# Optimization experiments

Hardware: AMD Instinct MI355X
Metric: run time of the kernel (lower is better)

Reference implementation:

```python
import jax, jax.numpy as jnp
import numpy as np

K = 131072
C = 128
THR = 9.2885e-30


def setup_inputs() -> dict:
    key = jax.random.key(0)
    k1, k2, k3, k4, k5 = jax.random.split(key, 5)
    scores1 = jax.random.normal(k1, (K, C), dtype=jnp.float32)
    scores2 = jax.random.normal(k2, (K, C), dtype=jnp.float32)
    # Build lineages hitting the three supported branches, never the
    # unsupported overlapping-but-unequal case (which raises in torch).
    c1 = jax.random.randint(k3, (K,), 0, C)
    off = jax.random.randint(k4, (K,), 1, C)
    c2 = (c1 + off) % C  # guaranteed != c1
    case = jax.random.randint(k5, (K,), 0, 3)  # 0: equal 1-hot, 1: equal 2-hot, 2: disjoint 1-hots
    oh1 = jax.nn.one_hot(c1, C, dtype=jnp.int32)
    oh2 = jax.nn.one_hot(c2, C, dtype=jnp.int32)
    is1 = (case == 1)[:, None]
    is2 = (case == 2)[:, None]
    Y1 = oh1 + jnp.where(is1, oh2, 0)
    Y2 = jnp.where(is2, oh2, Y1)
    return {"scores1": scores1, "Y1": Y1, "scores2": scores2, "Y2": Y2}


def reference(scores1, Y1, scores2, Y2):
    P1 = jax.nn.softmax(scores1, axis=1)  # [K, C]
    P2 = jax.nn.softmax(scores2, axis=1)
    L1 = Y1.astype(P1.dtype)
    L2 = Y2.astype(P2.dtype)

    eq = jnp.all(Y1 == Y2, axis=1)
    s = jnp.sum(Y1, axis=1)
    case1 = eq & (s == 1)   # equal one-hot lineage
    case2 = eq & (s == 2)   # equal two-hot lineage

    nclass = scores1.shape[1]
    rows = jnp.arange(scores1.shape[0])
    idx_a = jnp.argmax(Y1, axis=1)                      # first nonzero
    idx_b = nclass - 1 - jnp.argmax(Y1[:, ::-1], axis=1)  # last nonzero
    p1a = P1[rows, idx_a]; p1b = P1[rows, idx_b]
    p2a = P2[rows, idx_a]; p2b = P2[rows, idx_b]

    def safe_neglog(p):
        return jnp.where(p > THR, -jnp.log(jnp.maximum(p, THR)), 0.0)

    # case1: -log P1[i,c] - log P2[i,c] (each term thresholded)
    loss1 = safe_neglog(p1a) + safe_neglog(p2a)

    # case2: split two-hot into l1 (first pos), l2 (second pos); both one-hot
    # so disjunction == gathered prob.
    prob2 = 1.0 - (1.0 - p1a * p2b) * (1.0 - p1b * p2a)
    loss2 = safe_neglog(prob2)

    # default disjoint case: vectorized disjunction D(l,p) = 1 - prod(1 - l*p)
    D11 = 1.0 - jnp.prod(1.0 - L1 * P1, axis=1)  # Px1_Y1
    D21 = 1.0 - jnp.prod(1.0 - L2 * P1, axis=1)  # Px1_Y2
    D12 = 1.0 - jnp.prod(1.0 - L1 * P2, axis=1)  # Px2_Y1
    D22 = 1.0 - jnp.prod(1.0 - L2 * P2, axis=1)  # Px2_Y2
    probd = 1.0 - (1.0 - D11 * D22) * (1.0 - D21 * D12)
    lossd = safe_neglog(probd)

    return jnp.where(case1, loss1, jnp.where(case2, loss2, lossd))
```

## Files before the change

kernel.cpp:

```cpp
#include <hip/hip_runtime.h>


constexpr int KROWS = 131072;
constexpr int CC    = 128;
#define THRF 9.2885e-30f

__device__ __forceinline__ float hredsumf(float v){
#pragma unroll
  for (int m = 16; m > 0; m >>= 1) v += __shfl_xor(v, m, 32);
  return v;
}

__device__ __forceinline__ float neglog_safe(float p){
  return (p > THRF) ? -__logf(p) : 0.0f;
}

__device__ __forceinline__ float sel4(float p0, float p1, float p2, float p3, int s){
  float lo = (s & 1) ? p1 : p0;
  float hi = (s & 1) ? p3 : p2;
  return (s & 2) ? hi : lo;
}

__device__ __forceinline__ float gatherP(float p0, float p1, float p2, float p3, int idx){
  float c = sel4(p0, p1, p2, p3, idx & 3);
  return __shfl(c, (idx >> 2) & 31, 32);
}

__global__ __launch_bounds__(256) void wmc_loss_kernel(
    const float* __restrict__ s1, const int* __restrict__ y1,
    const float* __restrict__ s2, const int* __restrict__ y2,
    float* __restrict__ out)
{
  const int gid  = blockIdx.x * 256 + threadIdx.x;
  const int row  = gid >> 5;
  const int lane = threadIdx.x & 31;

  const size_t base = (size_t)row * CC;
  const float4 a1 = ((const float4*)(s1 + base))[lane];
  const float4 a2 = ((const float4*)(s2 + base))[lane];
  const int4   b1 = ((const int4*)(y1 + base))[lane];
  const int4   b2 = ((const int4*)(y2 + base))[lane];

  float e10 = __expf(a1.x), e11 = __expf(a1.y), e12 = __expf(a1.z), e13 = __expf(a1.w);
  float e20 = __expf(a2.x), e21 = __expf(a2.y), e22 = __expf(a2.z), e23 = __expf(a2.w);
  float inv1 = 1.0f / hredsumf(e10 + e11 + e12 + e13);
  float inv2 = 1.0f / hredsumf(e20 + e21 + e22 + e23);
  float p10 = e10 * inv1, p11 = e11 * inv1, p12 = e12 * inv1, p13 = e13 * inv1;
  float p20 = e20 * inv2, p21 = e21 * inv2, p22 = e22 * inv2, p23 = e23 * inv2;

  unsigned long long M1[4], M2[4];
  M1[0] = __ballot(b1.x); M1[1] = __ballot(b1.y); M1[2] = __ballot(b1.z); M1[3] = __ballot(b1.w);
  M2[0] = __ballot(b2.x); M2[1] = __ballot(b2.y); M2[2] = __ballot(b2.z); M2[3] = __ballot(b2.w);

  const bool hi = (threadIdx.x & 32) != 0;
  unsigned int h1[4], h2[4];
#pragma unroll
  for (int j = 0; j < 4; ++j) {
    h1[j] = hi ? (unsigned int)(M1[j] >> 32) : (unsigned int)M1[j];
    h2[j] = hi ? (unsigned int)(M2[j] >> 32) : (unsigned int)M2[j];
  }

  bool eq = (h1[0] == h2[0]) & (h1[1] == h2[1]) & (h1[2] == h2[2]) & (h1[3] == h2[3]);
  int srow = __popc(h1[0]) + __popc(h1[1]) + __popc(h1[2]) + __popc(h1[3]);

  int ia1 = 1 << 30, ib1 = -1, ia2 = 1 << 30, ib2 = -1;
#pragma unroll
  for (int j = 0; j < 4; ++j) {
    if (h1[j]) {
      ia1 = min(ia1, ((__ffs(h1[j]) - 1) << 2) + j);
      ib1 = max(ib1, ((31 - __clz(h1[j])) << 2) + j);
    }
    if (h2[j]) {
      ia2 = min(ia2, ((__ffs(h2[j]) - 1) << 2) + j);
      ib2 = max(ib2, ((31 - __clz(h2[j])) << 2) + j);
    }
  }

  float p1a1 = gatherP(p10, p11, p12, p13, ia1);
  float p1b1 = gatherP(p10, p11, p12, p13, ib1);
  float p1a2 = gatherP(p10, p11, p12, p13, ia2);
  float p1b2 = gatherP(p10, p11, p12, p13, ib2);
  float p2a1 = gatherP(p20, p21, p22, p23, ia1);
  float p2b1 = gatherP(p20, p21, p22, p23, ib1);
  float p2a2 = gatherP(p20, p21, p22, p23, ia2);
  float p2b2 = gatherP(p20, p21, p22, p23, ib2);

  float f1 = (ia1 != ib1) ? 1.0f : 0.0f;
  float f2 = (ia2 != ib2) ? 1.0f : 0.0f;
  float D11 = 1.0f - (1.0f - p1a1) * (1.0f - f1 * p1b1);
  float D12 = 1.0f - (1.0f - p2a1) * (1.0f - f1 * p2b1);
  float D21 = 1.0f - (1.0f - p1a2) * (1.0f - f2 * p1b2);
  float D22 = 1.0f - (1.0f - p2a2) * (1.0f - f2 * p2b2);

  float loss1 = neglog_safe(p1a1) + neglog_safe(p2a1);

  float prob2 = 1.0f - (1.0f - p1a1 * p2b1) * (1.0f - p1b1 * p2a1);
  float loss2 = neglog_safe(prob2);

  float probd = 1.0f - (1.0f - D11 * D22) * (1.0f - D21 * D12);
  float lossd = neglog_safe(probd);

  float loss = (eq && srow == 1) ? loss1 : (eq && srow == 2) ? loss2 : lossd;

  if (lane == 0) out[row] = loss;
}

extern "C" void kernel_launch(void* const* d_in, const int* in_sizes, int n_in,
                              void* d_out, int out_size, void* d_ws, size_t ws_size,
                              hipStream_t stream) {
  const float* s1 = (const float*)d_in[0];
  const int*   y1 = (const int*)d_in[1];
  const float* s2 = (const float*)d_in[2];
  const int*   y2 = (const int*)d_in[3];
  float* out = (float*)d_out;

  dim3 grid(KROWS / 8), block(256);
  wmc_loss_kernel<<<grid, block, 0, stream>>>(s1, y1, s2, y2, out);
}
```

Measured before the change: 232.8 us.

## Use persistent blocks with a software-prefetched row loop

The launch drops from one 8-row block per 256 threads (16384 blocks) to 2048 blocks, each looping over 8 iterations of 8 rows. The loads for the next row are issued before the current row is computed, so memory latency overlaps with compute. The aim is to cut block scheduling overhead and keep more loads in flight, at the cost of extra registers for the prefetched data and fewer, longer-lived blocks. The kernel is memory-bound and streams about 256MB, so bandwidth may already be saturated.

```diff
diff --git a/kernel.cpp b/kernel.cpp
--- a/kernel.cpp
+++ b/kernel.cpp
@@ -1,8 +1,11 @@
 #include <hip/hip_runtime.h>
 
 
-constexpr int KROWS = 131072;
-constexpr int CC    = 128;
+constexpr int KROWS       = 131072;
+constexpr int CC          = 128;
+constexpr int NB          = 2048;
+constexpr int ROWS_PER_IT = 8;
+constexpr int NIT         = KROWS / (NB * ROWS_PER_IT);
 #define THRF 9.2885e-30f
 
 __device__ __forceinline__ float hredsumf(float v){
@@ -26,21 +29,9 @@
   return __shfl(c, (idx >> 2) & 31, 32);
 }
 
-__global__ __launch_bounds__(256) void wmc_loss_kernel(
-    const float* __restrict__ s1, const int* __restrict__ y1,
-    const float* __restrict__ s2, const int* __restrict__ y2,
-    float* __restrict__ out)
+__device__ __forceinline__ float computeRow(
+    float4 a1, float4 a2, int4 b1, int4 b2, bool hi)
 {
-  const int gid  = blockIdx.x * 256 + threadIdx.x;
-  const int row  = gid >> 5;
-  const int lane = threadIdx.x & 31;
-
-  const size_t base = (size_t)row * CC;
-  const float4 a1 = ((const float4*)(s1 + base))[lane];
-  const float4 a2 = ((const float4*)(s2 + base))[lane];
-  const int4   b1 = ((const int4*)(y1 + base))[lane];
-  const int4   b2 = ((const int4*)(y2 + base))[lane];
-
   float e10 = __expf(a1.x), e11 = __expf(a1.y), e12 = __expf(a1.z), e13 = __expf(a1.w);
   float e20 = __expf(a2.x), e21 = __expf(a2.y), e22 = __expf(a2.z), e23 = __expf(a2.w);
   float inv1 = 1.0f / hredsumf(e10 + e11 + e12 + e13);
@@ -52,7 +43,6 @@
   M1[0] = __ballot(b1.x); M1[1] = __ballot(b1.y); M1[2] = __ballot(b1.z); M1[3] = __ballot(b1.w);
   M2[0] = __ballot(b2.x); M2[1] = __ballot(b2.y); M2[2] = __ballot(b2.z); M2[3] = __ballot(b2.w);
 
-  const bool hi = (threadIdx.x & 32) != 0;
   unsigned int h1[4], h2[4];
 #pragma unroll
   for (int j = 0; j < 4; ++j) {
@@ -93,16 +83,48 @@
   float D22 = 1.0f - (1.0f - p2a2) * (1.0f - f2 * p2b2);
 
   float loss1 = neglog_safe(p1a1) + neglog_safe(p2a1);
-
   float prob2 = 1.0f - (1.0f - p1a1 * p2b1) * (1.0f - p1b1 * p2a1);
   float loss2 = neglog_safe(prob2);
-
   float probd = 1.0f - (1.0f - D11 * D22) * (1.0f - D21 * D12);
   float lossd = neglog_safe(probd);
 
-  float loss = (eq && srow == 1) ? loss1 : (eq && srow == 2) ? loss2 : lossd;
+  return (eq && srow == 1) ? loss1 : (eq && srow == 2) ? loss2 : lossd;
+}
 
-  if (lane == 0) out[row] = loss;
+__global__ __launch_bounds__(256) void wmc_loss_kernel(
+    const float* __restrict__ s1, const int* __restrict__ y1,
+    const float* __restrict__ s2, const int* __restrict__ y2,
+    float* __restrict__ out)
+{
+  const int hw   = threadIdx.x >> 5;
+  const int lane = threadIdx.x & 31;
+  const bool hi  = (threadIdx.x & 32) != 0;
+  const int rowBase = blockIdx.x * (ROWS_PER_IT * NIT) + hw;
+
+  size_t base = (size_t)(rowBase) * CC;
+  float4 A1 = ((const float4*)(s1 + base))[lane];
+  float4 A2 = ((const float4*)(s2 + base))[lane];
+  int4   B1 = ((const int4*)(y1 + base))[lane];
+  int4   B2 = ((const int4*)(y2 + base))[lane];
+
+#pragma unroll
+  for (int it = 0; it < NIT; ++it) {
+    const int row = rowBase + it * ROWS_PER_IT;
+
+    float4 nA1, nA2; int4 nB1, nB2;
+    if (it + 1 < NIT) {
+      const size_t nbase = (size_t)(row + ROWS_PER_IT) * CC;
+      nA1 = ((const float4*)(s1 + nbase))[lane];
+      nA2 = ((const float4*)(s2 + nbase))[lane];
+      nB1 = ((const int4*)(y1 + nbase))[lane];
+      nB2 = ((const int4*)(y2 + nbase))[lane];
+    }
+
+    float loss = computeRow(A1, A2, B1, B2, hi);
+    if (lane == 0) out[row] = loss;
+
+    if (it + 1 < NIT) { A1 = nA1; A2 = nA2; B1 = nB1; B2 = nB2; }
+  }
 }
 
 extern "C" void kernel_launch(void* const* d_in, const int* in_sizes, int n_in,
@@ -114,6 +136,6 @@
   const int*   y2 = (const int*)d_in[3];
   float* out = (float*)d_out;
 
-  dim3 grid(KROWS / 8), block(256);
+  dim3 grid(NB), block(256);
   wmc_loss_kernel<<<grid, block, 0, stream>>>(s1, y1, s2, y2, out);
 }
```

After: 244.7 us. 1.05x slower.
